# Kernel optimization log

Hardware: AMD Instinct MI355X
Metric: run time of the kernel (lower is better)

Reference implementation:

```python
import jax, jax.numpy as jnp
import numpy as np

N = 100000       # num nodes
E = 1600000      # num edges (avg degree 16)
IN, HID, OUT, C = 128, 64, 64, 16


def setup_inputs() -> dict:
    key = jax.random.key(0)
    ks = jax.random.split(key, 10)
    x = jax.random.normal(ks[0], (N, IN), jnp.float32)
    edge_index = jax.random.randint(ks[1], (2, E), 0, N, dtype=jnp.int32)
    dict_node = jax.random.randint(ks[2], (N,), 0, N, dtype=jnp.int32)
    # learned parameters (Glorot-ish scaling)
    W1 = jax.random.normal(ks[3], (IN, HID), jnp.float32) / np.sqrt(IN)
    b1 = jnp.zeros((HID,), jnp.float32)
    W2 = jax.random.normal(ks[4], (HID, OUT), jnp.float32) / np.sqrt(HID)
    b2 = jnp.zeros((OUT,), jnp.float32)
    Wfc = jax.random.normal(ks[5], (OUT, C), jnp.float32) / np.sqrt(OUT)
    bfc = jnp.zeros((C,), jnp.float32)
    return {"x": x, "edge_index": edge_index, "dict_node": dict_node,
            "W1": W1, "b1": b1, "W2": W2, "b2": b2, "Wfc": Wfc, "bfc": bfc}


def _gcn_conv(h_in, W, b, src, dst, n):
    """GCNConv: D^-1/2 (A+I) D^-1/2 (X W) + b, self-loops handled analytically."""
    h = h_in @ W                                   # [N, F]
    deg = jax.ops.segment_sum(jnp.ones((src.shape[0],), h.dtype), dst,
                              num_segments=n) + 1.0  # +1 self-loop
    dinv = jax.lax.rsqrt(deg)                      # [N]
    norm = dinv[src] * dinv[dst]                   # [E]
    agg = jax.ops.segment_sum(h[src] * norm[:, None], dst, num_segments=n)
    agg = agg + h * (dinv * dinv)[:, None]         # self-loop contribution
    return agg + b


def reference(x, edge_index, dict_node, W1, b1, W2, b2, Wfc, bfc):
    n = x.shape[0]
    src, dst = edge_index[0], edge_index[1]
    h = jax.nn.relu(_gcn_conv(x, W1, b1, src, dst, n))
    # dropout p=0.5 is identity at inference
    h = jax.nn.relu(_gcn_conv(h, W2, b2, src, dst, n))
    # global_mean_pool over dict_node with size = num_nodes
    cnt = jax.ops.segment_sum(jnp.ones((n,), h.dtype), dict_node, num_segments=n)
    summ = jax.ops.segment_sum(h, dict_node, num_segments=n)
    pooled = summ / jnp.maximum(cnt, 1.0)[:, None]
    logits = pooled @ Wfc + bfc
    return jax.nn.log_softmax(logits, axis=1)
```

## Files before the change

kernel.cpp:

```cpp
#include <hip/hip_runtime.h>

#define THREADS 256
#define B1 256

typedef __attribute__((ext_vector_type(8))) short bf16x8;
typedef __attribute__((ext_vector_type(4))) float f32x4;
typedef __attribute__((ext_vector_type(2))) unsigned int u32x2;

__device__ inline ushort f2bf(float v) {
    union { float f; unsigned u; } a; a.f = v;
    unsigned r = a.u + 0x7fff + ((a.u >> 16) & 1);
    return (ushort)(r >> 16);
}
__device__ inline unsigned pack2(float a, float b) {
    return (unsigned)f2bf(a) | ((unsigned)f2bf(b) << 16);
}


__global__ void k_p1(const int* __restrict__ dst, int* __restrict__ pc,
                     int E, int NB, int chunk) {
    __shared__ int hist[512];
    int tid = threadIdx.x, blk = blockIdx.x;
    for (int i = tid; i < NB; i += THREADS) hist[i] = 0;
    __syncthreads();
    int e0 = blk * chunk;
    int e1 = e0 + chunk; if (e1 > E) e1 = E;
    for (int e = e0 + tid; e < e1; e += THREADS)
        atomicAdd(&hist[dst[e] >> 8], 1);
    __syncthreads();
    for (int i = tid; i < NB; i += THREADS) pc[i * B1 + blk] = hist[i];
}

__global__ void k_s1(int* __restrict__ pc, int* __restrict__ bsums, int total) {
    __shared__ int s[1024];
    int t = threadIdx.x;
    int idx = blockIdx.x * 1024 + t;
    int v = (idx < total) ? pc[idx] : 0;
    s[t] = v;
    __syncthreads();
    for (int o = 1; o < 1024; o <<= 1) {
        int x = (t >= (unsigned)o) ? s[t - o] : 0;
        __syncthreads();
        s[t] += x;
        __syncthreads();
    }
    if (idx < total) pc[idx] = s[t] - v;
    if (t == 1023) bsums[blockIdx.x] = s[1023];
}

__global__ void k_s2(int* __restrict__ bsums, int nb) {
    __shared__ int s[128];
    int t = threadIdx.x;
    int v = (t < nb) ? bsums[t] : 0;
    s[t] = v;
    __syncthreads();
    for (int o = 1; o < 128; o <<= 1) {
        int x = (t >= (unsigned)o) ? s[t - o] : 0;
        __syncthreads();
        s[t] += x;
        __syncthreads();
    }
    if (t < nb) bsums[t] = s[t] - v;
}

__global__ void k_p2(const int* __restrict__ src, const int* __restrict__ dst,
                     const int* __restrict__ pc, const int* __restrict__ bsx,
                     unsigned long long* __restrict__ part, int E, int NB, int chunk) {
    __shared__ int cur[512];
    int tid = threadIdx.x, blk = blockIdx.x;
    for (int i = tid; i < NB; i += THREADS) {
        int idx = i * B1 + blk;
        cur[i] = pc[idx] + bsx[idx >> 10];
    }
    __syncthreads();
    int e0 = blk * chunk;
    int e1 = e0 + chunk; if (e1 > E) e1 = E;
    for (int e = e0 + tid; e < e1; e += THREADS) {
        int d = dst[e], sv = src[e];
        int pos = atomicAdd(&cur[d >> 8], 1);
        part[pos] = ((unsigned long long)(unsigned)d << 32) | (unsigned)sv;
    }
}

__global__ void k_p3(const unsigned long long* __restrict__ part,
                     const int* __restrict__ pc, const int* __restrict__ bsx,
                     int* __restrict__ off, float* __restrict__ dinv,
                     int* __restrict__ csr, float* __restrict__ cnt,
                     int E, int NB, int n) {
    __shared__ int hist[256];
    __shared__ int so[256];
    int b = blockIdx.x, t = threadIdx.x;
    int i0 = b * B1, i1 = (b + 1) * B1;
    int base = pc[i0] + bsx[i0 >> 10];
    int end  = (b + 1 < NB) ? (pc[i1] + bsx[i1 >> 10]) : E;
    hist[t] = 0;
    __syncthreads();
    for (int e = base + t; e < end; e += THREADS)
        atomicAdd(&hist[(int)(part[e] >> 32) & 255], 1);
    __syncthreads();
    int h = hist[t];
    so[t] = h;
    __syncthreads();
    for (int o = 1; o < 256; o <<= 1) {
        int x = (t >= (unsigned)o) ? so[t - o] : 0;
        __syncthreads();
        so[t] += x;
        __syncthreads();
    }
    int ex = so[t] - h;
    int node = (b << 8) + t;
    if (node < n) {
        off[node]  = base + ex;
        dinv[node] = rsqrtf((float)h + 1.0f);
        cnt[node]  = 0.0f;
        if (node == n - 1) off[n] = E;
    }
    __syncthreads();
    so[t] = base + ex;
    __syncthreads();
    for (int e = base + t; e < end; e += THREADS) {
        unsigned long long p = part[e];
        int pos = atomicAdd(&so[(int)(p >> 32) & 255], 1);
        csr[pos] = (int)(p & 0xffffffffu);
    }
}

template<int KTILES, bool XF32>
__global__ __launch_bounds__(THREADS) void
k_mgemm(const float* __restrict__ Xf, const ushort* __restrict__ Xh,
        const float* __restrict__ W, const float* __restrict__ dinv,
        ushort* __restrict__ C, int n,
        const int* __restrict__ dict, float* __restrict__ cnt,
        float* __restrict__ pool16, int nGemm, int nCnt, int nZero) {
    int tid = threadIdx.x;
    if ((int)blockIdx.x >= nGemm) {
        int rb = (int)blockIdx.x - nGemm;
        if (rb < nCnt) {
            int stride = nCnt * THREADS;
            for (int i = rb * THREADS + tid; i < n; i += stride)
                atomicAdd(&cnt[dict[i]], 1.0f);
        } else {
            int zb = rb - nCnt;
            uint4* p4 = (uint4*)pool16;
            int tot = n * 4;
            int stride = nZero * THREADS;
            uint4 z = {0, 0, 0, 0};
            for (int i = zb * THREADS + tid; i < tot; i += stride) p4[i] = z;
        }
        return;
    }
    __shared__ ushort wfrag[KTILES * 2048];
    __shared__ float hrow[4][16 * 64];
    const int FIN = KTILES * 32;
    for (int i = tid; i < FIN * 64; i += THREADS) {
        int k = i >> 6, c = i & 63;
        int kk = k >> 5, G = (k >> 3) & 3, e = k & 7;
        int t = c >> 4, c16 = c & 15;
        wfrag[(((kk * 4 + t) * 64) + G * 16 + c16) * 8 + e] = f2bf(W[i]);
    }
    __syncthreads();
    int wslot = tid >> 6, lane = tid & 63;
    int G = lane >> 4, c16 = lane & 15;
    int n0 = blockIdx.x * 64 + wslot * 16;
    int xrow = n0 + c16; if (xrow >= n) xrow = n - 1;
    const bf16x8* wf = (const bf16x8*)wfrag;
    f32x4 acc0 = {0, 0, 0, 0}, acc1 = acc0, acc2 = acc0, acc3 = acc0;
    #pragma unroll
    for (int kk = 0; kk < KTILES; ++kk) {
        bf16x8 a;
        if (XF32) {
            const float* xp = Xf + (size_t)xrow * FIN + kk * 32 + G * 8;
            float4 xa = *(const float4*)xp;
            float4 xb = *(const float4*)(xp + 4);
            a[0] = (short)f2bf(xa.x); a[1] = (short)f2bf(xa.y);
            a[2] = (short)f2bf(xa.z); a[3] = (short)f2bf(xa.w);
            a[4] = (short)f2bf(xb.x); a[5] = (short)f2bf(xb.y);
            a[6] = (short)f2bf(xb.z); a[7] = (short)f2bf(xb.w);
        } else {
            a = *(const bf16x8*)(Xh + (size_t)xrow * FIN + kk * 32 + G * 8);
        }
        bf16x8 b0 = wf[(kk * 4 + 0) * 64 + lane];
        bf16x8 b1 = wf[(kk * 4 + 1) * 64 + lane];
        bf16x8 b2 = wf[(kk * 4 + 2) * 64 + lane];
        bf16x8 b3 = wf[(kk * 4 + 3) * 64 + lane];
        acc0 = __builtin_amdgcn_mfma_f32_16x16x32_bf16(a, b0, acc0, 0, 0, 0);
        acc1 = __builtin_amdgcn_mfma_f32_16x16x32_bf16(a, b1, acc1, 0, 0, 0);
        acc2 = __builtin_amdgcn_mfma_f32_16x16x32_bf16(a, b2, acc2, 0, 0, 0);
        acc3 = __builtin_amdgcn_mfma_f32_16x16x32_bf16(a, b3, acc3, 0, 0, 0);
    }
    int vm = n - n0; if (vm > 16) vm = 16;
    float* hr = &hrow[wslot][0];
    #pragma unroll
    for (int r = 0; r < 4; ++r) {
        int rr = G * 4 + r;
        if (rr < vm) {
            float dn = dinv[n0 + rr];
            hr[rr * 64 + c16]      = acc0[r] * dn;
            hr[rr * 64 + c16 + 16] = acc1[r] * dn;
            hr[rr * 64 + c16 + 32] = acc2[r] * dn;
            hr[rr * 64 + c16 + 48] = acc3[r] * dn;
        }
    }
    asm volatile("" ::: "memory");
    int prow = lane >> 2, pseg = lane & 3;
    if (prow < vm) {
        const float* hp = hr + prow * 64 + pseg * 16;
        float4 f0 = *(const float4*)(hp + 0);
        float4 f1 = *(const float4*)(hp + 4);
        float4 f2 = *(const float4*)(hp + 8);
        float4 f3 = *(const float4*)(hp + 12);
        uint4 o0, o1;
        o0.x = pack2(f0.x, f0.y); o0.y = pack2(f0.z, f0.w);
        o0.z = pack2(f1.x, f1.y); o0.w = pack2(f1.z, f1.w);
        o1.x = pack2(f2.x, f2.y); o1.y = pack2(f2.z, f2.w);
        o1.z = pack2(f3.x, f3.y); o1.w = pack2(f3.z, f3.w);
        ushort* op = C + ((size_t)(n0 + prow) << 6) + pseg * 16;
        *(uint4*)(op)     = o0;
        *(uint4*)(op + 8) = o1;
    }
}

__device__ inline void tr_mfma4(unsigned la, const bf16x8& a,
                                f32x4& o0, f32x4& o1, f32x4& o2, f32x4& o3) {
    u32x2 r0, r1, r2, r3, r4, r5, r6, r7;
    asm volatile(
        "s_waitcnt lgkmcnt(0)\n\t"
        "ds_read_b64_tr_b16 %0, %8 offset:0\n\t"
        "ds_read_b64_tr_b16 %1, %8 offset:512\n\t"
        "ds_read_b64_tr_b16 %2, %8 offset:1024\n\t"
        "ds_read_b64_tr_b16 %3, %8 offset:1536\n\t"
        "ds_read_b64_tr_b16 %4, %8 offset:2048\n\t"
        "ds_read_b64_tr_b16 %5, %8 offset:2560\n\t"
        "ds_read_b64_tr_b16 %6, %8 offset:3072\n\t"
        "ds_read_b64_tr_b16 %7, %8 offset:3584\n\t"
        "s_waitcnt lgkmcnt(0)"
        : "=&v"(r0), "=&v"(r1), "=&v"(r2), "=&v"(r3),
          "=&v"(r4), "=&v"(r5), "=&v"(r6), "=&v"(r7)
        : "v"(la) : "memory");
    __builtin_amdgcn_sched_barrier(0);
    union { u32x2 d[2]; bf16x8 v; } b0, b1, b2, b3;
    b0.d[0] = r0; b0.d[1] = r1; b1.d[0] = r2; b1.d[1] = r3;
    b2.d[0] = r4; b2.d[1] = r5; b3.d[0] = r6; b3.d[1] = r7;
    o0 = __builtin_amdgcn_mfma_f32_16x16x32_bf16(a, b0.v, o0, 0, 0, 0);
    o1 = __builtin_amdgcn_mfma_f32_16x16x32_bf16(a, b1.v, o1, 0, 0, 0);
    o2 = __builtin_amdgcn_mfma_f32_16x16x32_bf16(a, b2.v, o2, 0, 0, 0);
    o3 = __builtin_amdgcn_mfma_f32_16x16x32_bf16(a, b3.v, o3, 0, 0, 0);
}

template<int LAYER>
__global__ __launch_bounds__(THREADS) void
k_agg(const ushort* __restrict__ H, const int* __restrict__ csr,
      const int* __restrict__ off, const float* __restrict__ dinv,
      const float* __restrict__ bias, ushort* __restrict__ outB,
      const float* __restrict__ Wfc, const int* __restrict__ dict,
      float* __restrict__ pool16, int n) {
    __shared__ ushort cbuf[4][2048];
    __shared__ float wt[16 * 65];
    int tid = threadIdx.x;
    if (LAYER == 2) {
        for (int i = tid; i < 64 * 16; i += THREADS) {
            int cc = i >> 4, r = i & 15;
            wt[r * 65 + cc] = Wfc[i];
        }
        __syncthreads();
    }
    int wslot = tid >> 6, lane = tid & 63;
    int gw = blockIdx.x * 4 + wslot;
    int n0 = gw << 4;
    if (n0 >= n) return;
    int G = lane >> 4, c16 = lane & 15;
    int g8 = lane >> 3, q = lane & 7;
    ushort* wbuf = &cbuf[wslot][0];
    unsigned lbase = (unsigned)(size_t)wbuf;
    int vm = n - n0; if (vm > 16) vm = 16;
    int sA = 0, eA = 0;
    if (c16 < vm) { sA = off[n0 + c16]; eA = off[n0 + c16 + 1]; }
    int base0   = __shfl(sA, 0);
    int baseEnd = __shfl(eA, vm - 1);
    unsigned rng = (unsigned)(eA - sA);
    int sb0 = (q >> 1) * 512 + (g8 >> 2) * 256 + (g8 & 3) * 16 + (q & 1) * 8;
    unsigned la = lbase + (unsigned)lane * 8;
    f32x4 acc0 = {0, 0, 0, 0}, acc1 = acc0, acc2 = acc0, acc3 = acc0;

    uint4 c0[4], c1[4], c2[4];
    #pragma unroll
    for (int it = 0; it < 4; ++it) {
        uint4 v = {0, 0, 0, 0};
        int k = base0 + it * 8 + g8;
        if (k < baseEnd) {
            int e = csr[k];
            v = *(const uint4*)(H + ((size_t)e << 6) + q * 8);
        }
        c0[it] = v;
    }
    #pragma unroll
    for (int it = 0; it < 4; ++it) {
        uint4 v = {0, 0, 0, 0};
        int k = base0 + 32 + it * 8 + g8;
        if (k < baseEnd) {
            int e = csr[k];
            v = *(const uint4*)(H + ((size_t)e << 6) + q * 8);
        }
        c1[it] = v;
    }
    for (int base = base0; base < baseEnd; base += 32) {
        #pragma unroll
        for (int it = 0; it < 4; ++it) {
            uint4 v = {0, 0, 0, 0};
            int k = base + 64 + it * 8 + g8;
            if (k < baseEnd) {
                int e = csr[k];
                v = *(const uint4*)(H + ((size_t)e << 6) + q * 8);
            }
            c2[it] = v;
        }
        #pragma unroll
        for (int it = 0; it < 4; ++it)
            *(uint4*)(wbuf + sb0 + it * 64) = c0[it];
        int kb = base - sA;
        bf16x8 a;
        #pragma unroll
        for (int e2 = 0; e2 < 8; ++e2)
            a[e2] = ((unsigned)(G * 8 + e2 + kb) < rng) ? (short)0x3F80 : (short)0;
        tr_mfma4(la, a, acc0, acc1, acc2, acc3);
        #pragma unroll
        for (int it = 0; it < 4; ++it) { c0[it] = c1[it]; c1[it] = c2[it]; }
    }
    {
        #pragma unroll
        for (int it = 0; it < 4; ++it) {
            uint4 v = {0, 0, 0, 0};
            int k = it * 8 + g8;
            if (it < 2 && k < vm)
                v = *(const uint4*)(H + ((size_t)(n0 + k) << 6) + q * 8);
            *(uint4*)(wbuf + sb0 + it * 64) = v;
        }
        bf16x8 a;
        #pragma unroll
        for (int e2 = 0; e2 < 8; ++e2)
            a[e2] = ((G * 8 + e2) == c16) ? (short)0x3F80 : (short)0;
        tr_mfma4(la, a, acc0, acc1, acc2, acc3);
    }
    float* hrow = (float*)wbuf;
    float bv0 = bias[c16], bv1 = bias[c16 + 16],
          bv2 = bias[c16 + 32], bv3 = bias[c16 + 48];
    #pragma unroll
    for (int r = 0; r < 4; ++r) {
        int rr = G * 4 + r;
        if (rr < vm) {
            float dn = dinv[n0 + rr];
            float v0 = fmaxf(acc0[r] * dn + bv0, 0.f);
            float v1 = fmaxf(acc1[r] * dn + bv1, 0.f);
            float v2 = fmaxf(acc2[r] * dn + bv2, 0.f);
            float v3 = fmaxf(acc3[r] * dn + bv3, 0.f);
            hrow[rr * 64 + c16]      = v0;
            hrow[rr * 64 + c16 + 16] = v1;
            hrow[rr * 64 + c16 + 32] = v2;
            hrow[rr * 64 + c16 + 48] = v3;
        }
    }
    asm volatile("" ::: "memory");
    if (LAYER == 1) {
        int prow = lane >> 2, pseg = lane & 3;
        if (prow < vm) {
            const float* hp = hrow + prow * 64 + pseg * 16;
            float4 f0 = *(const float4*)(hp + 0);
            float4 f1 = *(const float4*)(hp + 4);
            float4 f2 = *(const float4*)(hp + 8);
            float4 f3 = *(const float4*)(hp + 12);
            uint4 o0, o1;
            o0.x = pack2(f0.x, f0.y); o0.y = pack2(f0.z, f0.w);
            o0.z = pack2(f1.x, f1.y); o0.w = pack2(f1.z, f1.w);
            o1.x = pack2(f2.x, f2.y); o1.y = pack2(f2.z, f2.w);
            o1.z = pack2(f3.x, f3.y); o1.w = pack2(f3.z, f3.w);
            ushort* op = outB + ((size_t)(n0 + prow) << 6) + pseg * 16;
            *(uint4*)(op)     = o0;
            *(uint4*)(op + 8) = o1;
        }
    } else {
        int r16 = c16;
        for (int m = 0; m < vm; ++m) {
            const float* hm = hrow + m * 64 + G * 16;
            const float* wr = wt + r16 * 65 + G * 16;
            float p = 0.f;
            #pragma unroll
            for (int i = 0; i < 16; ++i) p = fmaf(hm[i], wr[i], p);
            p += __shfl_xor(p, 16);
            p += __shfl_xor(p, 32);
            if (G == 0)
                atomicAdd(&pool16[(size_t)dict[n0 + m] * 16 + r16], p);
        }
    }
}

__global__ void k_final16(const float* __restrict__ pool16, const float* __restrict__ cnt,
                          const float* __restrict__ bfc, float* __restrict__ out, int n) {
    int tid = threadIdx.x;
    int nl = tid >> 4, lane = tid & 15;
    int node = blockIdx.x * 16 + nl;
    if (node >= n) return;
    float inv = 1.0f / fmaxf(cnt[node], 1.0f);
    float acc = pool16[(size_t)node * 16 + lane] * inv + bfc[lane];
    float m = acc;
    for (int o = 8; o; o >>= 1) m = fmaxf(m, __shfl_xor(m, o, 16));
    float ex = __expf(acc - m);
    float s = ex;
    for (int o = 8; o; o >>= 1) s += __shfl_xor(s, o, 16);
    out[(size_t)node * 16 + lane] = acc - m - __logf(s);
}

extern "C" void kernel_launch(void* const* d_in, const int* in_sizes, int n_in,
                              void* d_out, int out_size, void* d_ws, size_t ws_size,
                              hipStream_t stream) {
    const float* x    = (const float*)d_in[0];
    const int*   ei   = (const int*)d_in[1];
    const int*   dict = (const int*)d_in[2];
    const float* W1   = (const float*)d_in[3];
    const float* b1   = (const float*)d_in[4];
    const float* W2   = (const float*)d_in[5];
    const float* b2   = (const float*)d_in[6];
    const float* Wfc  = (const float*)d_in[7];
    const float* bfc  = (const float*)d_in[8];

    const int N  = in_sizes[2];
    const int E  = in_sizes[1] / 2;
    const int IN = in_sizes[0] / N;
    const int* src = ei;
    const int* dst = ei + E;

    ushort* bufA = (ushort*)d_ws;
    ushort* bufB = bufA + (size_t)N * 64;
    unsigned long long* part = (unsigned long long*)bufB;
    float* dinv    = (float*)(bufB + (size_t)N * 64);
    float* cnt     = dinv + N;
    int*   off     = (int*)(cnt + N);
    int*   pcounts = off + (N + 1);
    const int NB     = (N + 255) >> 8;
    const int pcsize = NB * B1;
    int*   bsums   = pcounts + pcsize;
    int*   csr     = bsums + 128;
    float* pool16  = (float*)(csr + E);

    const int gTile = (N + 63) / 64;
    const int gRows = (N + 15) / 16;
    const int nCnt  = 256;
    const int nZero = 256;
    const int chunk = (E + B1 - 1) / B1;
    const int nS1   = (pcsize + 1023) >> 10;
    const int gAgg  = ((N + 15) / 16 + 3) / 4;

    k_p1<<<B1, THREADS, 0, stream>>>(dst, pcounts, E, NB, chunk);
    k_s1<<<nS1, 1024, 0, stream>>>(pcounts, bsums, pcsize);
    k_s2<<<1, 128, 0, stream>>>(bsums, nS1);
    k_p2<<<B1, THREADS, 0, stream>>>(src, dst, pcounts, bsums, part, E, NB, chunk);
    k_p3<<<NB, THREADS, 0, stream>>>(part, pcounts, bsums, off, dinv, csr, cnt,
                                     E, NB, N);

    k_mgemm<4, true><<<gTile + nCnt + nZero, THREADS, 0, stream>>>(
        x, nullptr, W1, dinv, bufA, N, dict, cnt, pool16, gTile, nCnt, nZero);

    k_agg<1><<<gAgg, THREADS, 0, stream>>>(bufA, csr, off, dinv, b1, bufB,
                                           nullptr, nullptr, nullptr, N);

    k_mgemm<2, false><<<gTile, THREADS, 0, stream>>>(
        nullptr, bufB, W2, dinv, bufA, N, nullptr, nullptr, nullptr, gTile, 0, 0);
    k_agg<2><<<gAgg, THREADS, 0, stream>>>(bufA, csr, off, dinv, b2, nullptr,
                                           Wfc, dict, pool16, N);

    k_final16<<<gRows, THREADS, 0, stream>>>(pool16, cnt, bfc, (float*)d_out, N);
}
```

Before: 280.9 us.

## Fuse layer-2 feature transform GEMM into layer-1 aggregation epilogue

The layer-1 aggregation kernel now loads W2 into shared memory as bf16 in MFMA fragment layout and, after computing relu(agg+b1), multiplies the 16-row tile by W2 with MFMA, scales by dinv and writes the pre-scaled layer-2 input directly. The separate k_mgemm<2> launch and its read/write round-trip of the hidden activations are removed. This adds LDS usage and epilogue work to the aggregation kernel, which may lower occupancy.

Result: faster. 271.2 us, median of 2 (-3.4%).

```diff
diff --git a/kernel.cpp b/kernel.cpp
--- a/kernel.cpp
+++ b/kernel.cpp
@@ -252,15 +252,24 @@
 k_agg(const ushort* __restrict__ H, const int* __restrict__ csr,
       const int* __restrict__ off, const float* __restrict__ dinv,
       const float* __restrict__ bias, ushort* __restrict__ outB,
-      const float* __restrict__ Wfc, const int* __restrict__ dict,
+      const float* __restrict__ wsrc, const int* __restrict__ dict,
       float* __restrict__ pool16, int n) {
     __shared__ ushort cbuf[4][2048];
-    __shared__ float wt[16 * 65];
+    __shared__ ushort extra[LAYER == 1 ? 4096 : 2080];
     int tid = threadIdx.x;
-    if (LAYER == 2) {
+    if (LAYER == 1) {
+        for (int i = tid; i < 64 * 64; i += THREADS) {
+            int k = i >> 6, c = i & 63;
+            int kk = k >> 5, Gs = (k >> 3) & 3, e = k & 7;
+            int t = c >> 4, cs = c & 15;
+            extra[(((kk * 4 + t) * 64) + Gs * 16 + cs) * 8 + e] = f2bf(wsrc[i]);
+        }
+        __syncthreads();
+    } else {
+        float* wt = (float*)extra;
         for (int i = tid; i < 64 * 16; i += THREADS) {
             int cc = i >> 4, r = i & 15;
-            wt[r * 65 + cc] = Wfc[i];
+            wt[r * 65 + cc] = wsrc[i];
         }
         __syncthreads();
     }
@@ -361,6 +370,43 @@
     }
     asm volatile("" ::: "memory");
     if (LAYER == 1) {
+        const float* ap = hrow + c16 * 64 + G * 8;
+        float4 xa = *(const float4*)(ap);
+        float4 xb = *(const float4*)(ap + 4);
+        float4 ya = *(const float4*)(ap + 32);
+        float4 yb = *(const float4*)(ap + 36);
+        bf16x8 a0, a1;
+        a0[0] = (short)f2bf(xa.x); a0[1] = (short)f2bf(xa.y);
+        a0[2] = (short)f2bf(xa.z); a0[3] = (short)f2bf(xa.w);
+        a0[4] = (short)f2bf(xb.x); a0[5] = (short)f2bf(xb.y);
+        a0[6] = (short)f2bf(xb.z); a0[7] = (short)f2bf(xb.w);
+        a1[0] = (short)f2bf(ya.x); a1[1] = (short)f2bf(ya.y);
+        a1[2] = (short)f2bf(ya.z); a1[3] = (short)f2bf(ya.w);
+        a1[4] = (short)f2bf(yb.x); a1[5] = (short)f2bf(yb.y);
+        a1[6] = (short)f2bf(yb.z); a1[7] = (short)f2bf(yb.w);
+        const bf16x8* wf2 = (const bf16x8*)extra;
+        f32x4 h0 = {0, 0, 0, 0}, h1v = h0, h2v = h0, h3v = h0;
+        h0  = __builtin_amdgcn_mfma_f32_16x16x32_bf16(a0, wf2[0 * 64 + lane], h0, 0, 0, 0);
+        h1v = __builtin_amdgcn_mfma_f32_16x16x32_bf16(a0, wf2[1 * 64 + lane], h1v, 0, 0, 0);
+        h2v = __builtin_amdgcn_mfma_f32_16x16x32_bf16(a0, wf2[2 * 64 + lane], h2v, 0, 0, 0);
+        h3v = __builtin_amdgcn_mfma_f32_16x16x32_bf16(a0, wf2[3 * 64 + lane], h3v, 0, 0, 0);
+        h0  = __builtin_amdgcn_mfma_f32_16x16x32_bf16(a1, wf2[4 * 64 + lane], h0, 0, 0, 0);
+        h1v = __builtin_amdgcn_mfma_f32_16x16x32_bf16(a1, wf2[5 * 64 + lane], h1v, 0, 0, 0);
+        h2v = __builtin_amdgcn_mfma_f32_16x16x32_bf16(a1, wf2[6 * 64 + lane], h2v, 0, 0, 0);
+        h3v = __builtin_amdgcn_mfma_f32_16x16x32_bf16(a1, wf2[7 * 64 + lane], h3v, 0, 0, 0);
+        asm volatile("" ::: "memory");
+        #pragma unroll
+        for (int r = 0; r < 4; ++r) {
+            int rr = G * 4 + r;
+            if (rr < vm) {
+                float dn = dinv[n0 + rr];
+                hrow[rr * 64 + c16]      = h0[r] * dn;
+                hrow[rr * 64 + c16 + 16] = h1v[r] * dn;
+                hrow[rr * 64 + c16 + 32] = h2v[r] * dn;
+                hrow[rr * 64 + c16 + 48] = h3v[r] * dn;
+            }
+        }
+        asm volatile("" ::: "memory");
         int prow = lane >> 2, pseg = lane & 3;
         if (prow < vm) {
             const float* hp = hrow + prow * 64 + pseg * 16;
@@ -378,6 +424,7 @@
             *(uint4*)(op + 8) = o1;
         }
     } else {
+        const float* wt = (const float*)extra;
         int r16 = c16;
         for (int m = 0; m < vm; ++m) {
             const float* hm = hrow + m * 64 + G * 16;
@@ -460,11 +507,9 @@
         x, nullptr, W1, dinv, bufA, N, dict, cnt, pool16, gTile, nCnt, nZero);
 
     k_agg<1><<<gAgg, THREADS, 0, stream>>>(bufA, csr, off, dinv, b1, bufB,
-                                           nullptr, nullptr, nullptr, N);
-
-    k_mgemm<2, false><<<gTile, THREADS, 0, stream>>>(
-        nullptr, bufB, W2, dinv, bufA, N, nullptr, nullptr, nullptr, gTile, 0, 0);
-    k_agg<2><<<gAgg, THREADS, 0, stream>>>(bufA, csr, off, dinv, b2, nullptr,
+                                           W2, nullptr, nullptr, N);
+
+    k_agg<2><<<gAgg, THREADS, 0, stream>>>(bufB, csr, off, dinv, b2, nullptr,
                                            Wfc, dict, pool16, N);
 
     k_final16<<<gRows, THREADS, 0, stream>>>(pool16, cnt, bfc, (float*)d_out, N);
```
